# Optimization experiments

Hardware: AMD Instinct MI355X
Metric: run time of the kernel (lower is better)

## Reference

```python
import jax, jax.numpy as jnp
import numpy as np

B, N, C = 8, 4096, 3
IN_DIM = 2
HID = 512
NL = 256          # num_latents
DEPTH = 6
H, DH = 8, 64     # heads, dim_head (cross and latent)
INNER = H * DH
LAT = 32          # latent (bottleneck) dim
NF, MAXF = 12, 4  # NeRF num_freq, max_freq_log2
FF = 4 * HID
SCALE = DH ** -0.5
NERF_DIM = 2 * NF * IN_DIM  # 48


def layer_norm(x, g, b, eps=1e-5):
    m = jnp.mean(x, axis=-1, keepdims=True)
    v = jnp.mean((x - m) ** 2, axis=-1, keepdims=True)
    return (x - m) * jax.lax.rsqrt(v + eps) * g + b


def nerf_encode(pos):
    # log-sampled frequency bands: 2^linspace(0, MAXF, NF)
    freqs = 2.0 ** jnp.linspace(0.0, float(MAXF), NF)
    ang = pos[..., None] * freqs            # [B,N,IN_DIM,NF]
    enc = jnp.concatenate([jnp.sin(ang), jnp.cos(ang)], axis=-1)  # [B,N,IN_DIM,2NF]
    return enc.reshape(*pos.shape[:-1], NERF_DIM)


def mha(q, k, v):
    # q:[B,Nq,INNER] k,v:[B,Nk,INNER] -> [B,Nq,INNER]
    def split(t):
        b, n, _ = t.shape
        return t.reshape(b, n, H, DH).transpose(0, 2, 1, 3)  # [B,H,n,DH]
    qh, kh, vh = split(q), split(k), split(v)
    sim = jnp.einsum('bhid,bhjd->bhij', qh, kh) * SCALE
    attn = jax.nn.softmax(sim, axis=-1)
    o = jnp.einsum('bhij,bhjd->bhid', attn, vh)
    return o.transpose(0, 2, 1, 3).reshape(q.shape[0], q.shape[1], INNER)


def setup_inputs():
    key = jax.random.key(0)
    ks = iter(jax.random.split(key, 64))
    def w(*shape):
        return jax.random.normal(next(ks), shape, jnp.float32) * 0.02
    inp = {}
    inp['x'] = jax.random.normal(next(ks), (B, N, C), jnp.float32)
    inp['pos'] = jax.random.uniform(next(ks), (B, N, IN_DIM), jnp.float32)
    # input embeddings
    inp['W_pos'] = w(NERF_DIM, HID); inp['b_pos'] = jnp.zeros((HID,), jnp.float32)
    inp['W_in'] = w(C, HID); inp['b_in'] = jnp.zeros((HID,), jnp.float32)
    inp['latents'] = w(NL, HID)
    # cross-attention (PreNormCross: norm on q, k, v)
    for n in ('lnq', 'lnk', 'lnv'):
        inp[n + '_g'] = jnp.ones((HID,), jnp.float32)
        inp[n + '_b'] = jnp.zeros((HID,), jnp.float32)
    inp['cWq'] = w(HID, INNER); inp['cWk'] = w(HID, INNER); inp['cWv'] = w(HID, INNER)
    inp['cWo'] = w(INNER, HID); inp['c_bo'] = jnp.zeros((HID,), jnp.float32)
    # self-attention + FFN stacks
    inp['ln1_g'] = jnp.ones((DEPTH, HID), jnp.float32); inp['ln1_b'] = jnp.zeros((DEPTH, HID), jnp.float32)
    inp['sWq'] = w(DEPTH, HID, INNER); inp['sWkv'] = w(DEPTH, HID, 2 * INNER)
    inp['sWo'] = w(DEPTH, INNER, HID); inp['s_bo'] = jnp.zeros((DEPTH, HID), jnp.float32)
    inp['ln2_g'] = jnp.ones((DEPTH, HID), jnp.float32); inp['ln2_b'] = jnp.zeros((DEPTH, HID), jnp.float32)
    inp['fW1'] = w(DEPTH, HID, FF); inp['f_b1'] = jnp.zeros((DEPTH, FF), jnp.float32)
    inp['fW2'] = w(DEPTH, FF, HID); inp['f_b2'] = jnp.zeros((DEPTH, HID), jnp.float32)
    # final norm + gaussian bottleneck projection (mean, logvar)
    inp['lnf_g'] = jnp.ones((HID,), jnp.float32); inp['lnf_b'] = jnp.zeros((HID,), jnp.float32)
    inp['Wb'] = w(HID, 2 * LAT); inp['bb'] = jnp.zeros((2 * LAT,), jnp.float32)
    return inp


def reference(x, pos, W_pos, b_pos, W_in, b_in, latents,
              lnq_g, lnq_b, lnk_g, lnk_b, lnv_g, lnv_b,
              cWq, cWk, cWv, cWo, c_bo,
              ln1_g, ln1_b, sWq, sWkv, sWo, s_bo,
              ln2_g, ln2_b, fW1, f_b1, fW2, f_b2,
              lnf_g, lnf_b, Wb, bb):
    # positional embedding (FourierPositionalEmbedding with relu)
    kin = jax.nn.relu(nerf_encode(pos) @ W_pos + b_pos)   # [B,N,HID]
    vin = x @ W_in + b_in                                 # [B,N,HID]
    vin = vin + kin                                       # include_pos_in_value
    lat = jnp.broadcast_to(latents, (B, NL, HID))
    # cross-attention block (PreNormCross + residual)
    qn = layer_norm(lat, lnq_g, lnq_b)
    kn = layer_norm(kin, lnk_g, lnk_b)
    vn = layer_norm(vin, lnv_g, lnv_b)
    o = mha(qn @ cWq, kn @ cWk, vn @ cWv) @ cWo + c_bo
    lat = lat + o
    # latent self-attention + FFN blocks
    for i in range(DEPTH):
        h1 = layer_norm(lat, ln1_g[i], ln1_b[i])
        q = h1 @ sWq[i]
        k, v = jnp.split(h1 @ sWkv[i], 2, axis=-1)
        lat = lat + (mha(q, k, v) @ sWo[i] + s_bo[i])
        h2 = layer_norm(lat, ln2_g[i], ln2_b[i])
        lat = lat + (jax.nn.gelu(h2 @ fW1[i] + f_b1[i]) @ fW2[i] + f_b2[i])
    # bottleneck projection -> (mean | logvar)
    out = layer_norm(lat, lnf_g, lnf_b) @ Wb + bb         # [B,NL,2*LAT]
    return out
```

## Files before the change

### kernel.cpp

```cpp
#include <hip/hip_runtime.h>
#include <hip/hip_bf16.h>

#define DEV __device__ __forceinline__

typedef __attribute__((ext_vector_type(8))) short short8;
typedef __attribute__((ext_vector_type(4))) float floatx4;

DEV short f2bf(float f) {
  unsigned u = __float_as_uint(f);
  u += 0x7fffu + ((u >> 16) & 1u);
  return (short)(u >> 16);
}
DEV float bf2f(short s) {
  return __uint_as_float(((unsigned)(unsigned short)s) << 16);
}
DEV float wred(float v) {
#pragma unroll
  for (int m = 1; m < 64; m <<= 1) v += __shfl_xor(v, m);
  return v;
}
DEV floatx4 mfma16(short8 a, short8 b, floatx4 c) {
  return __builtin_amdgcn_mfma_f32_16x16x32_bf16(a, b, c, 0, 0, 0);
}
DEV void gload16(void* lds, const void* g) {
  __builtin_amdgcn_global_load_lds(
      (const __attribute__((address_space(1))) unsigned int*)g,
      (__attribute__((address_space(3))) unsigned int*)lds, 16, 0, 0);
}

struct MatDesc { const float* src; int K; int N; int kp; int off; float scale; };
struct MatTable { MatDesc m[36]; };

__global__ __launch_bounds__(256) void wtrans_kernel(MatTable T, short* __restrict__ dst) {
  int mi = blockIdx.y;
  MatDesc d = T.m[mi];
  int tilesx = d.N >> 5, tilesy = d.kp >> 5;
  int tb = blockIdx.x;
  if (tb >= tilesx * tilesy) return;
  int ty = tb / tilesx, tx = tb % tilesx;
  __shared__ float tile[32][33];
  int tid = threadIdx.x;
#pragma unroll
  for (int i = 0; i < 4; ++i) {
    int e = tid + i * 256, lr = e >> 5, lc = e & 31;
    int kk = ty * 32 + lr;
    tile[lr][lc] = (kk < d.K) ? d.src[(size_t)kk * d.N + tx * 32 + lc] : 0.f;
  }
  __syncthreads();
#pragma unroll
  for (int i = 0; i < 4; ++i) {
    int e = tid + i * 256, lr = e >> 5, lc = e & 31;
    dst[(size_t)d.off + (size_t)(tx * 32 + lr) * d.kp + ty * 32 + lc] =
        f2bf(tile[lc][lr] * d.scale);
  }
}

__global__ __launch_bounds__(256) void enc_kernel(const float* __restrict__ pos,
                                                  short* __restrict__ enc) {
  int idx = blockIdx.x * 256 + threadIdx.x;
  int row = idx >> 3, oct = idx & 7;
  float p0 = pos[row * 2], p1 = pos[row * 2 + 1];
  short8 o;
#pragma unroll
  for (int j = 0; j < 8; ++j) {
    int k = oct * 8 + j;
    float val = 0.f;
    if (k < 48) {
      int dd = k / 24, rem = k % 24;
      int trig = rem / 12, f = rem % 12;
      float ang = (dd ? p1 : p0) * exp2f((4.0f / 11.0f) * (float)f);
      val = trig ? __cosf(ang) : __sinf(ang);
    }
    o[j] = f2bf(val);
  }
  *(short8*)&enc[(size_t)row * 64 + oct * 8] = o;
}

#define LDA_S 516
__global__ __launch_bounds__(512) void embed2_kernel(
    const short* __restrict__ enc, const short* __restrict__ Wt,
    const float* __restrict__ b_pos, const float* __restrict__ W_in,
    const float* __restrict__ b_in, const float* __restrict__ x,
    const float* __restrict__ lnk_g, const float* __restrict__ lnk_b,
    const float* __restrict__ lnv_g, const float* __restrict__ lnv_b,
    short* __restrict__ kn, short* __restrict__ vn) {
  __shared__ short SS[128 * LDA_S];
  short* Wl = SS;
  short* El = SS + 32768;
  int tid = threadIdx.x;
  int lane = tid & 63, wv = tid >> 6;
  int c = lane & 15, g = lane >> 4;
  int blk = blockIdx.x * 128;
#pragma unroll
  for (int gi = 0; gi < 8; ++gi) {
    int grp = wv * 8 + gi;
    int row = grp * 8 + (lane >> 3), kc = lane & 7;
    gload16(&Wl[grp * 512], &Wt[(size_t)row * 64 + ((kc ^ (row & 7)) * 8)]);
  }
#pragma unroll
  for (int gi = 0; gi < 2; ++gi) {
    int grp = wv * 2 + gi;
    int row = grp * 8 + (lane >> 3), kc = lane & 7;
    gload16(&El[grp * 512], &enc[(size_t)(blk + row) * 64 + ((kc ^ (row & 7)) * 8)]);
  }
  __syncthreads();

  floatx4 acc[32];
  floatx4 zf = {0.f, 0.f, 0.f, 0.f};
#pragma unroll
  for (int nf = 0; nf < 32; ++nf) acc[nf] = zf;
  short8 af[2];
#pragma unroll
  for (int ks = 0; ks < 2; ++ks)
    af[ks] = *(const short8*)&El[(wv * 16 + c) * 64 + ((ks * 4 + g) ^ (c & 7)) * 8];
#pragma unroll
  for (int nf = 0; nf < 32; ++nf) {
#pragma unroll
    for (int ks = 0; ks < 2; ++ks) {
      short8 bf8 = *(const short8*)&Wl[(nf * 16 + c) * 64 + ((ks * 4 + g) ^ (c & 7)) * 8];
      acc[nf] = mfma16(af[ks], bf8, acc[nf]);
    }
  }

  int rowbase = blk + wv * 16 + g * 4;
  int lrow = wv * 16 + g * 4;
  float x0[4], x1[4], x2[4];
  float s1[4], q1[4], s2[4], q2[4];
#pragma unroll
  for (int r = 0; r < 4; ++r) {
    x0[r] = x[(size_t)(rowbase + r) * 3];
    x1[r] = x[(size_t)(rowbase + r) * 3 + 1];
    x2[r] = x[(size_t)(rowbase + r) * 3 + 2];
    s1[r] = 0; q1[r] = 0; s2[r] = 0; q2[r] = 0;
  }
#pragma unroll
  for (int nf = 0; nf < 32; ++nf) {
    int col = nf * 16 + c;
    float bp = b_pos[col];
    float w0 = W_in[col], w1 = W_in[512 + col], w2 = W_in[1024 + col], bi = b_in[col];
#pragma unroll
    for (int r = 0; r < 4; ++r) {
      float kk = fmaxf(acc[nf][r] + bp, 0.f);
      float vv = kk + x0[r] * w0 + x1[r] * w1 + x2[r] * w2 + bi;
      acc[nf][r] = kk;
      s1[r] += kk; q1[r] += kk * kk; s2[r] += vv; q2[r] += vv * vv;
    }
  }
  float m1[4], r1[4], m2[4], r2[4];
#pragma unroll
  for (int r = 0; r < 4; ++r) {
#pragma unroll
    for (int msk = 1; msk < 16; msk <<= 1) {
      s1[r] += __shfl_xor(s1[r], msk); q1[r] += __shfl_xor(q1[r], msk);
      s2[r] += __shfl_xor(s2[r], msk); q2[r] += __shfl_xor(q2[r], msk);
    }
    m1[r] = s1[r] * (1.f / 512.f);
    r1[r] = rsqrtf(q1[r] * (1.f / 512.f) - m1[r] * m1[r] + 1e-5f);
    m2[r] = s2[r] * (1.f / 512.f);
    r2[r] = rsqrtf(q2[r] * (1.f / 512.f) - m2[r] * m2[r] + 1e-5f);
  }
  __syncthreads();
#pragma unroll
  for (int nf = 0; nf < 32; ++nf) {
    int col = nf * 16 + c;
    float gk = lnk_g[col], bk = lnk_b[col];
#pragma unroll
    for (int r = 0; r < 4; ++r)
      SS[(lrow + r) * LDA_S + col] = f2bf((acc[nf][r] - m1[r]) * r1[r] * gk + bk);
  }
  __syncthreads();
#pragma unroll
  for (int it = 0; it < 16; ++it) {
    int e = it * 512 + tid;
    int row = e >> 6, colc = (e & 63) * 8;
    *(short8*)&kn[(size_t)(blk + row) * 512 + colc] = *(const short8*)&SS[row * LDA_S + colc];
  }
  __syncthreads();
#pragma unroll
  for (int nf = 0; nf < 32; ++nf) {
    int col = nf * 16 + c;
    float w0 = W_in[col], w1 = W_in[512 + col], w2 = W_in[1024 + col], bi = b_in[col];
    float gv = lnv_g[col], bv = lnv_b[col];
#pragma unroll
    for (int r = 0; r < 4; ++r) {
      float vv = acc[nf][r] + x0[r] * w0 + x1[r] * w1 + x2[r] * w2 + bi;
      SS[(lrow + r) * LDA_S + col] = f2bf((vv - m2[r]) * r2[r] * gv + bv);
    }
  }
  __syncthreads();
#pragma unroll
  for (int it = 0; it < 16; ++it) {
    int e = it * 512 + tid;
    int row = e >> 6, colc = (e & 63) * 8;
    *(short8*)&vn[(size_t)(blk + row) * 512 + colc] = *(const short8*)&SS[row * LDA_S + colc];
  }
}

__global__ __launch_bounds__(256) void ln_kernel(
    const float* __restrict__ in, const float* __restrict__ g,
    const float* __restrict__ b, short* __restrict__ out, int M) {
  int row = blockIdx.x * 4 + (threadIdx.x >> 6);
  if (row >= M) return;
  int lane = threadIdx.x & 63;
  float v[8]; float s = 0, q = 0;
#pragma unroll
  for (int j = 0; j < 8; ++j) {
    v[j] = in[(size_t)row * 512 + lane + 64 * j];
    s += v[j]; q += v[j] * v[j];
  }
  s = wred(s); q = wred(q);
  float m = s * (1.f / 512.f);
  float rs = rsqrtf(q * (1.f / 512.f) - m * m + 1e-5f);
#pragma unroll
  for (int j = 0; j < 8; ++j) {
    int cc = lane + 64 * j;
    out[(size_t)row * 512 + cc] = f2bf((v[j] - m) * rs * g[cc] + b[cc]);
  }
}

__global__ void bcast_kernel(const float* __restrict__ latents, float* __restrict__ lat) {
  int i = blockIdx.x * 256 + threadIdx.x;
  lat[i] = latents[i & 131071];
}

template <int EPI>
DEV void epi_store(void* outp, size_t idx, float xv) {
  if (EPI == 0) {
    ((short*)outp)[idx] = f2bf(xv);
  } else if (EPI == 1) {
    float t = 0.7978845608f * (xv + 0.044715f * xv * xv * xv);
    ((short*)outp)[idx] = f2bf(0.5f * xv * (1.f + tanhf(t)));
  } else if (EPI == 2) {
    ((float*)outp)[idx] += xv;
  } else {
    ((float*)outp)[idx] = xv;
  }
}

template <int EPI>
__global__ __launch_bounds__(256) void gemm_kernel(
    const short* __restrict__ A, const short* __restrict__ Wt,
    const float* __restrict__ bias, void* __restrict__ outp,
    int M, int N, int K, int lda, int ldo) {
  __shared__ short Alds[128 * 64];
  __shared__ short Blds[128 * 64];
  int tid = threadIdx.x;
  int brow = blockIdx.y * 128, bcol = blockIdx.x * 128;
  int lane = tid & 63, wvid = tid >> 6;
  int wr = wvid >> 1, wc = wvid & 1;
  int g = lane >> 4, c = lane & 15;
  floatx4 zf = {0.f, 0.f, 0.f, 0.f};
  floatx4 acc[4][4];
#pragma unroll
  for (int i = 0; i < 4; ++i)
#pragma unroll
    for (int j = 0; j < 4; ++j) acc[i][j] = zf;

  int srow = (lane >> 3), skc = lane & 7;
  for (int k0 = 0; k0 < K; k0 += 64) {
#pragma unroll
    for (int gi = 0; gi < 4; ++gi) {
      int grp = wvid * 4 + gi;
      int row = grp * 8 + srow;
      int sw = ((skc ^ (row & 7)) * 8);
      gload16(&Alds[grp * 512], &A[(size_t)(brow + row) * lda + k0 + sw]);
      gload16(&Blds[grp * 512], &Wt[(size_t)(bcol + row) * K + k0 + sw]);
    }
    __syncthreads();
#pragma unroll
    for (int ks = 0; ks < 2; ++ks) {
      int slot = ((ks * 4 + g) ^ (c & 7)) * 8;
      short8 af[4], bf8[4];
#pragma unroll
      for (int mf = 0; mf < 4; ++mf)
        af[mf] = *(const short8*)&Alds[(wr * 64 + mf * 16 + c) * 64 + slot];
#pragma unroll
      for (int nf = 0; nf < 4; ++nf)
        bf8[nf] = *(const short8*)&Blds[(wc * 64 + nf * 16 + c) * 64 + slot];
#pragma unroll
      for (int mf = 0; mf < 4; ++mf)
#pragma unroll
        for (int nf = 0; nf < 4; ++nf)
          acc[mf][nf] = mfma16(af[mf], bf8[nf], acc[mf][nf]);
    }
    __syncthreads();
  }

#pragma unroll
  for (int mf = 0; mf < 4; ++mf) {
#pragma unroll
    for (int nf = 0; nf < 4; ++nf) {
      int col = bcol + wc * 64 + nf * 16 + c;
      float bv = bias ? bias[col] : 0.f;
      int row0 = brow + wr * 64 + mf * 16 + g * 4;
#pragma unroll
      for (int r = 0; r < 4; ++r)
        epi_store<EPI>(outp, (size_t)(row0 + r) * ldo + col, acc[mf][nf][r] + bv);
    }
  }
}

template <int EPI>
__global__ __launch_bounds__(256) void gemm64_kernel(
    const short* __restrict__ A, const short* __restrict__ Wt,
    const float* __restrict__ bias, void* __restrict__ outp,
    int M, int N, int K, int lda, int ldo) {
  __shared__ short Alds[64 * 64];
  __shared__ short Blds[64 * 64];
  int tid = threadIdx.x;
  int brow = blockIdx.y * 64, bcol = blockIdx.x * 64;
  int lane = tid & 63, wvid = tid >> 6;
  int wr = wvid >> 1, wc = wvid & 1;
  int g = lane >> 4, c = lane & 15;
  floatx4 zf = {0.f, 0.f, 0.f, 0.f};
  floatx4 acc[2][2];
#pragma unroll
  for (int i = 0; i < 2; ++i)
#pragma unroll
    for (int j = 0; j < 2; ++j) acc[i][j] = zf;

  int srow = (lane >> 3), skc = lane & 7;
  for (int k0 = 0; k0 < K; k0 += 64) {
#pragma unroll
    for (int gi = 0; gi < 2; ++gi) {
      int grp = wvid * 2 + gi;
      int row = grp * 8 + srow;
      int sw = ((skc ^ (row & 7)) * 8);
      gload16(&Alds[grp * 512], &A[(size_t)(brow + row) * lda + k0 + sw]);
      gload16(&Blds[grp * 512], &Wt[(size_t)(bcol + row) * K + k0 + sw]);
    }
    __syncthreads();
#pragma unroll
    for (int ks = 0; ks < 2; ++ks) {
      int slot = ((ks * 4 + g) ^ (c & 7)) * 8;
      short8 af[2], bf8[2];
#pragma unroll
      for (int mf = 0; mf < 2; ++mf)
        af[mf] = *(const short8*)&Alds[(wr * 32 + mf * 16 + c) * 64 + slot];
#pragma unroll
      for (int nf = 0; nf < 2; ++nf)
        bf8[nf] = *(const short8*)&Blds[(wc * 32 + nf * 16 + c) * 64 + slot];
#pragma unroll
      for (int mf = 0; mf < 2; ++mf)
#pragma unroll
        for (int nf = 0; nf < 2; ++nf)
          acc[mf][nf] = mfma16(af[mf], bf8[nf], acc[mf][nf]);
    }
    __syncthreads();
  }

#pragma unroll
  for (int mf = 0; mf < 2; ++mf) {
#pragma unroll
    for (int nf = 0; nf < 2; ++nf) {
      int col = bcol + wc * 32 + nf * 16 + c;
      float bv = bias ? bias[col] : 0.f;
      int row0 = brow + wr * 32 + mf * 16 + g * 4;
#pragma unroll
      for (int r = 0; r < 4; ++r)
        epi_store<EPI>(outp, (size_t)(row0 + r) * ldo + col, acc[mf][nf][r] + bv);
    }
  }
}

__global__ __launch_bounds__(512) void flashsp_kernel(
    const short* __restrict__ q, const short* __restrict__ k,
    const short* __restrict__ v, float* __restrict__ po,
    float* __restrict__ pm, float* __restrict__ pl,
    int qrs, int qbrows, long kvbstride, int kvrstride,
    int seglen, int lognseg) {
  __shared__ short Qs[128 * 64];
  __shared__ short Ks[64 * 64];
  __shared__ short Vt[64 * 72];
  __shared__ short Ps[128 * 72];
  int tid = threadIdx.x;
  int bz = blockIdx.z;
  int b = bz >> lognseg, seg = bz & ((1 << lognseg) - 1);
  int h = blockIdx.y, qt = blockIdx.x;
  int lane = tid & 63, wv = tid >> 6;
  int g = lane >> 4, c = lane & 15;
  int srow = lane >> 3, skc = lane & 7;

#pragma unroll
  for (int gi = 0; gi < 2; ++gi) {
    int grp = wv * 2 + gi;
    int row = grp * 8 + srow;
    int sw = ((skc ^ (row & 7)) * 8);
    gload16(&Qs[grp * 512],
            &q[((size_t)(b * qbrows) + qt * 128 + row) * qrs + h * 64 + sw]);
  }

  float m_[4], l_[4];
  floatx4 zf = {0.f, 0.f, 0.f, 0.f};
  floatx4 o_[4];
#pragma unroll
  for (int r = 0; r < 4; ++r) { m_[r] = -3.0e38f; l_[r] = 0.f; }
#pragma unroll
  for (int f = 0; f < 4; ++f) o_[f] = zf;

  int tbeg = seg * seglen, tend = tbeg + seglen;
  for (int t0 = tbeg; t0 < tend; t0 += 64) {
    {
      int row = wv * 8 + srow;
      int sw = ((skc ^ (row & 7)) * 8);
      gload16(&Ks[wv * 512],
              &k[(size_t)b * kvbstride + (size_t)(t0 + row) * kvrstride + h * 64 + sw]);
    }
    {
      int j = tid >> 3, f0 = (tid & 7) * 8, mm = tid & 7, tg = j >> 3;
      short8 tv = *(const short8*)&v[(size_t)b * kvbstride + (size_t)(t0 + j) * kvrstride + h * 64 + f0];
#pragma unroll
      for (int jj = 0; jj < 8; ++jj)
        Vt[(f0 + jj) * 72 + ((tg ^ mm) * 8) + (j & 7)] = tv[jj];
    }
    __syncthreads();

    floatx4 s[4];
#pragma unroll
    for (int f = 0; f < 4; ++f) s[f] = zf;
#pragma unroll
    for (int ks = 0; ks < 2; ++ks) {
      int slot = ((ks * 4 + g) ^ (c & 7)) * 8;
      short8 a = *(const short8*)&Qs[(wv * 16 + c) * 64 + slot];
#pragma unroll
      for (int f = 0; f < 4; ++f) {
        short8 b8 = *(const short8*)&Ks[(f * 16 + c) * 64 + slot];
        s[f] = mfma16(a, b8, s[f]);
      }
    }

    float nm[4], sf[4], rs[4];
#pragma unroll
    for (int r = 0; r < 4; ++r) {
      float t = fmaxf(fmaxf(s[0][r], s[1][r]), fmaxf(s[2][r], s[3][r]));
#pragma unroll
      for (int msk = 1; msk < 16; msk <<= 1) t = fmaxf(t, __shfl_xor(t, msk));
      nm[r] = fmaxf(m_[r], t);
      sf[r] = __expf(m_[r] - nm[r]);
      rs[r] = 0.f;
    }
#pragma unroll
    for (int f = 0; f < 4; ++f)
#pragma unroll
      for (int r = 0; r < 4; ++r) {
        float p = __expf(s[f][r] - nm[r]);
        s[f][r] = p; rs[r] += p;
      }
#pragma unroll
    for (int r = 0; r < 4; ++r) {
#pragma unroll
      for (int msk = 1; msk < 16; msk <<= 1) rs[r] += __shfl_xor(rs[r], msk);
      l_[r] = l_[r] * sf[r] + rs[r];
      m_[r] = nm[r];
    }
#pragma unroll
    for (int f = 0; f < 4; ++f)
#pragma unroll
      for (int r = 0; r < 4; ++r) o_[f][r] *= sf[r];
#pragma unroll
    for (int f = 0; f < 4; ++f)
#pragma unroll
      for (int r = 0; r < 4; ++r)
        Ps[(wv * 16 + g * 4 + r) * 72 + f * 16 + c] = f2bf(s[f][r]);
    __syncthreads();
#pragma unroll
    for (int ks = 0; ks < 2; ++ks) {
      short8 pa = *(const short8*)&Ps[(wv * 16 + c) * 72 + ks * 32 + g * 8];
#pragma unroll
      for (int f = 0; f < 4; ++f) {
        int mm = (2 * f + (c >> 3)) & 7;
        short8 vb = *(const short8*)&Vt[(f * 16 + c) * 72 + ((ks * 4 + g) ^ mm) * 8];
        o_[f] = mfma16(pa, vb, o_[f]);
      }
    }
    __syncthreads();
  }

#pragma unroll
  for (int f = 0; f < 4; ++f)
#pragma unroll
    for (int r = 0; r < 4; ++r) {
      int row = qt * 128 + wv * 16 + g * 4 + r;
      size_t grow = (size_t)seg * 2048 + b * 256 + row;
      po[grow * 512 + h * 64 + f * 16 + c] = o_[f][r];
      if (f == 0 && c == 0) {
        pm[grow * 8 + h] = m_[r];
        pl[grow * 8 + h] = l_[r];
      }
    }
}

template <int NSEG>
__global__ __launch_bounds__(256) void fcomb_kernel(
    const float* __restrict__ po, const float* __restrict__ pm,
    const float* __restrict__ pl, short* __restrict__ out) {
  int idx = blockIdx.x * 256 + threadIdx.x;
  int grow = idx >> 9, col = idx & 511, h = col >> 6;
  float ms[NSEG];
  float M = -3.0e38f;
#pragma unroll
  for (int s = 0; s < NSEG; ++s) {
    ms[s] = pm[((size_t)s * 2048 + grow) * 8 + h];
    M = fmaxf(M, ms[s]);
  }
  float L = 0.f, acc = 0.f;
#pragma unroll
  for (int s = 0; s < NSEG; ++s) {
    float w = __expf(ms[s] - M);
    L += w * pl[((size_t)s * 2048 + grow) * 8 + h];
    acc += w * po[((size_t)s * 2048 + grow) * 512 + col];
  }
  out[idx] = f2bf(acc / L);
}

extern "C" void kernel_launch(void* const* d_in, const int* in_sizes, int n_in,
                              void* d_out, int out_size, void* d_ws, size_t ws_size,
                              hipStream_t stream) {
  const float* x       = (const float*)d_in[0];
  const float* pos     = (const float*)d_in[1];
  const float* W_pos   = (const float*)d_in[2];
  const float* b_pos   = (const float*)d_in[3];
  const float* W_in    = (const float*)d_in[4];
  const float* b_in    = (const float*)d_in[5];
  const float* latents = (const float*)d_in[6];
  const float* lnq_g   = (const float*)d_in[7];
  const float* lnq_b   = (const float*)d_in[8];
  const float* lnk_g   = (const float*)d_in[9];
  const float* lnk_b   = (const float*)d_in[10];
  const float* lnv_g   = (const float*)d_in[11];
  const float* lnv_b   = (const float*)d_in[12];
  const float* cWq     = (const float*)d_in[13];
  const float* cWk     = (const float*)d_in[14];
  const float* cWv     = (const float*)d_in[15];
  const float* cWo     = (const float*)d_in[16];
  const float* c_bo    = (const float*)d_in[17];
  const float* ln1_g   = (const float*)d_in[18];
  const float* ln1_b   = (const float*)d_in[19];
  const float* sWq     = (const float*)d_in[20];
  const float* sWkv    = (const float*)d_in[21];
  const float* sWo     = (const float*)d_in[22];
  const float* s_bo    = (const float*)d_in[23];
  const float* ln2_g   = (const float*)d_in[24];
  const float* ln2_b   = (const float*)d_in[25];
  const float* fW1     = (const float*)d_in[26];
  const float* f_b1    = (const float*)d_in[27];
  const float* fW2     = (const float*)d_in[28];
  const float* f_b2    = (const float*)d_in[29];
  const float* lnf_g   = (const float*)d_in[30];
  const float* lnf_b   = (const float*)d_in[31];
  const float* Wb      = (const float*)d_in[32];
  const float* bbv     = (const float*)d_in[33];
  float* outp = (float*)d_out;

  size_t W = 0;
  size_t o_cWq = W; W += 512 * 512;
  size_t o_cWk = W; W += 512 * 512;
  size_t o_cWv = W; W += 512 * 512;
  size_t o_cWo = W; W += 512 * 512;
  size_t o_Wb  = W; W += 64 * 512;
  size_t o_Wpos = W; W += 512 * 64;
  size_t o_sQKV[6], o_sWo[6], o_fW1[6], o_fW2[6];
  for (int i = 0; i < 6; ++i) {
    o_sQKV[i] = W; W += 1536 * 512;
    o_sWo[i]  = W; W += 512 * 512;
    o_fW1[i]  = W; W += 2048 * 512;
    o_fW2[i]  = W; W += 512 * 2048;
  }
  MatTable T;
  int nm = 0;
  auto add = [&](const float* s, int K, int N, int kp, size_t off, float sc) {
    T.m[nm].src = s; T.m[nm].K = K; T.m[nm].N = N; T.m[nm].kp = kp;
    T.m[nm].off = (int)off; T.m[nm].scale = sc; ++nm;
  };
  const float SC = 0.125f;
  add(cWq, 512, 512, 512, o_cWq, SC); add(cWk, 512, 512, 512, o_cWk, 1.f);
  add(cWv, 512, 512, 512, o_cWv, 1.f); add(cWo, 512, 512, 512, o_cWo, 1.f);
  add(Wb, 512, 64, 512, o_Wb, 1.f);
  add(W_pos, 48, 512, 64, o_Wpos, 1.f);
  for (int i = 0; i < 6; ++i) {
    add(sWq  + (size_t)i * 512 * 512,  512, 512,  512, o_sQKV[i], SC);
    add(sWkv + (size_t)i * 512 * 1024, 512, 1024, 512, o_sQKV[i] + 512 * 512, 1.f);
    add(sWo  + (size_t)i * 512 * 512,  512, 512,  512, o_sWo[i], 1.f);
    add(fW1  + (size_t)i * 512 * 2048, 512, 2048, 512, o_fW1[i], 1.f);
    add(fW2  + (size_t)i * 2048 * 512, 2048, 512, 2048, o_fW2[i], 1.f);
  }

  char* p = (char*)d_ws;
  auto carve = [&](size_t bytes) {
    char* r = p; p += (bytes + 255) & ~(size_t)255; return r;
  };
  short* wtb   = (short*)carve(W * 2);
  short* enc   = (short*)carve((size_t)32768 * 64 * 2);
  short* kn    = (short*)carve(33554432);
  short* vn    = (short*)carve(33554432);
  short* kvc   = (short*)carve((size_t)32768 * 1024 * 2);
  short* latn0 = (short*)carve(262144);
  short* qc    = (short*)carve(262144);
  float* lat   = (float*)carve(4194304);
  float* pm    = (float*)carve(1048576);
  float* pl    = (float*)carve(1048576);
  short* attno = enc;
  float* po    = (float*)kn;
  short* h     = (short*)((char*)kn + 36 * 1048576);
  short* qkv   = (short*)((char*)kn + 40 * 1048576);
  short* ffh   = (short*)((char*)kn + 48 * 1048576);

  wtrans_kernel<<<dim3(1024, 36), 256, 0, stream>>>(T, wtb);
  enc_kernel<<<1024, 256, 0, stream>>>(pos, enc);
  embed2_kernel<<<256, 512, 0, stream>>>(enc, wtb + o_Wpos, b_pos, W_in, b_in, x,
                                         lnk_g, lnk_b, lnv_g, lnv_b, kn, vn);
  bcast_kernel<<<4096, 256, 0, stream>>>(latents, lat);
  ln_kernel<<<64, 256, 0, stream>>>(latents, lnq_g, lnq_b, latn0, 256);
  gemm64_kernel<0><<<dim3(8, 4), 256, 0, stream>>>(latn0, wtb + o_cWq, nullptr, qc, 256, 512, 512, 512, 512);
  gemm_kernel<0><<<dim3(4, 256), 256, 0, stream>>>(kn, wtb + o_cWk, nullptr, kvc, 32768, 512, 512, 512, 1024);
  gemm_kernel<0><<<dim3(4, 256), 256, 0, stream>>>(vn, wtb + o_cWv, nullptr, kvc + 512, 32768, 512, 512, 512, 1024);
  flashsp_kernel<<<dim3(2, 8, 64), 512, 0, stream>>>(qc, kvc, kvc + 512, po, pm, pl,
                                                     512, 0, (long)4096 * 1024, 1024, 512, 3);
  fcomb_kernel<8><<<4096, 256, 0, stream>>>(po, pm, pl, attno);
  gemm64_kernel<2><<<dim3(8, 32), 256, 0, stream>>>(attno, wtb + o_cWo, c_bo, lat, 2048, 512, 512, 512, 512);

  for (int i = 0; i < 6; ++i) {
    ln_kernel<<<512, 256, 0, stream>>>(lat, ln1_g + i * 512, ln1_b + i * 512, h, 2048);
    gemm64_kernel<0><<<dim3(24, 32), 256, 0, stream>>>(h, wtb + o_sQKV[i], nullptr, qkv, 2048, 1536, 512, 512, 1536);
    flashsp_kernel<<<dim3(2, 8, 32), 512, 0, stream>>>(qkv, qkv + 512, qkv + 1024, po, pm, pl,
                                                       1536, 256, (long)256 * 1536, 1536, 64, 2);
    fcomb_kernel<4><<<4096, 256, 0, stream>>>(po, pm, pl, attno);
    gemm64_kernel<2><<<dim3(8, 32), 256, 0, stream>>>(attno, wtb + o_sWo[i], s_bo + i * 512, lat, 2048, 512, 512, 512, 512);
    ln_kernel<<<512, 256, 0, stream>>>(lat, ln2_g + i * 512, ln2_b + i * 512, h, 2048);
    gemm64_kernel<1><<<dim3(32, 32), 256, 0, stream>>>(h, wtb + o_fW1[i], f_b1 + i * 2048, ffh, 2048, 2048, 512, 512, 2048);
    gemm64_kernel<2><<<dim3(8, 32), 256, 0, stream>>>(ffh, wtb + o_fW2[i], f_b2 + i * 512, lat, 2048, 512, 2048, 2048, 512);
  }
  ln_kernel<<<512, 256, 0, stream>>>(lat, lnf_g, lnf_b, h, 2048);
  gemm64_kernel<3><<<dim3(1, 32), 256, 0, stream>>>(h, wtb + o_Wb, bbv, outp, 2048, 64, 512, 512, 64);
}
```

Baseline: 822.6 us.

## Fuse LayerNorm into GEMM A-loads and shrink embed LDS staging buffer

Adds a gemm64ln kernel that computes per-row LayerNorm statistics from the fp32 input, then normalizes and converts A tiles to bf16 on the fly while loading them into LDS. This removes the separate ln_kernel launches and the bf16 intermediate round trips before the Q, QKV, FFN1 and bottleneck GEMMs. Each block recomputes the row stats and rereads fp32 A instead of bf16, which is redundant work across column blocks. The embed kernel also stages its output in two 64-row halves so it uses a smaller LDS buffer, which could allow higher occupancy, at the cost of extra barriers.

```diff
diff --git a/kernel.cpp b/kernel.cpp
--- a/kernel.cpp
+++ b/kernel.cpp
@@ -13,11 +13,6 @@
 }
 DEV float bf2f(short s) {
   return __uint_as_float(((unsigned)(unsigned short)s) << 16);
-}
-DEV float wred(float v) {
-#pragma unroll
-  for (int m = 1; m < 64; m <<= 1) v += __shfl_xor(v, m);
-  return v;
 }
 DEV floatx4 mfma16(short8 a, short8 b, floatx4 c) {
   return __builtin_amdgcn_mfma_f32_16x16x32_bf16(a, b, c, 0, 0, 0);
@@ -76,7 +71,7 @@
   *(short8*)&enc[(size_t)row * 64 + oct * 8] = o;
 }
 
-#define LDA_S 516
+#define LDA_S 528
 __global__ __launch_bounds__(512) void embed2_kernel(
     const short* __restrict__ enc, const short* __restrict__ Wt,
     const float* __restrict__ b_pos, const float* __restrict__ W_in,
@@ -84,7 +79,7 @@
     const float* __restrict__ lnk_g, const float* __restrict__ lnk_b,
     const float* __restrict__ lnv_g, const float* __restrict__ lnv_b,
     short* __restrict__ kn, short* __restrict__ vn) {
-  __shared__ short SS[128 * LDA_S];
+  __shared__ short SS[40960];
   short* Wl = SS;
   short* El = SS + 32768;
   int tid = threadIdx.x;
@@ -123,7 +118,6 @@
   }
 
   int rowbase = blk + wv * 16 + g * 4;
-  int lrow = wv * 16 + g * 4;
   float x0[4], x1[4], x2[4];
   float s1[4], q1[4], s2[4], q2[4];
 #pragma unroll
@@ -159,62 +153,55 @@
     m2[r] = s2[r] * (1.f / 512.f);
     r2[r] = rsqrtf(q2[r] * (1.f / 512.f) - m2[r] * m2[r] + 1e-5f);
   }
-  __syncthreads();
-#pragma unroll
-  for (int nf = 0; nf < 32; ++nf) {
-    int col = nf * 16 + c;
-    float gk = lnk_g[col], bk = lnk_b[col];
-#pragma unroll
-    for (int r = 0; r < 4; ++r)
-      SS[(lrow + r) * LDA_S + col] = f2bf((acc[nf][r] - m1[r]) * r1[r] * gk + bk);
-  }
-  __syncthreads();
-#pragma unroll
-  for (int it = 0; it < 16; ++it) {
-    int e = it * 512 + tid;
-    int row = e >> 6, colc = (e & 63) * 8;
-    *(short8*)&kn[(size_t)(blk + row) * 512 + colc] = *(const short8*)&SS[row * LDA_S + colc];
-  }
-  __syncthreads();
-#pragma unroll
-  for (int nf = 0; nf < 32; ++nf) {
-    int col = nf * 16 + c;
-    float w0 = W_in[col], w1 = W_in[512 + col], w2 = W_in[1024 + col], bi = b_in[col];
-    float gv = lnv_g[col], bv = lnv_b[col];
-#pragma unroll
-    for (int r = 0; r < 4; ++r) {
-      float vv = acc[nf][r] + x0[r] * w0 + x1[r] * w1 + x2[r] * w2 + bi;
-      SS[(lrow + r) * LDA_S + col] = f2bf((vv - m2[r]) * r2[r] * gv + bv);
-    }
-  }
-  __syncthreads();
-#pragma unroll
-  for (int it = 0; it < 16; ++it) {
-    int e = it * 512 + tid;
-    int row = e >> 6, colc = (e & 63) * 8;
-    *(short8*)&vn[(size_t)(blk + row) * 512 + colc] = *(const short8*)&SS[row * LDA_S + colc];
-  }
-}
-
-__global__ __launch_bounds__(256) void ln_kernel(
-    const float* __restrict__ in, const float* __restrict__ g,
-    const float* __restrict__ b, short* __restrict__ out, int M) {
-  int row = blockIdx.x * 4 + (threadIdx.x >> 6);
-  if (row >= M) return;
-  int lane = threadIdx.x & 63;
-  float v[8]; float s = 0, q = 0;
-#pragma unroll
-  for (int j = 0; j < 8; ++j) {
-    v[j] = in[(size_t)row * 512 + lane + 64 * j];
-    s += v[j]; q += v[j] * v[j];
-  }
-  s = wred(s); q = wred(q);
-  float m = s * (1.f / 512.f);
-  float rs = rsqrtf(q * (1.f / 512.f) - m * m + 1e-5f);
-#pragma unroll
-  for (int j = 0; j < 8; ++j) {
-    int cc = lane + 64 * j;
-    out[(size_t)row * 512 + cc] = f2bf((v[j] - m) * rs * g[cc] + b[cc]);
+
+  int halfsel = wv >> 2;
+  int lrow = (wv & 3) * 16 + g * 4;
+#pragma unroll
+  for (int half = 0; half < 2; ++half) {
+    __syncthreads();
+    if (halfsel == half) {
+#pragma unroll
+      for (int nf = 0; nf < 32; ++nf) {
+        int col = nf * 16 + c;
+        float gk = lnk_g[col], bk = lnk_b[col];
+#pragma unroll
+        for (int r = 0; r < 4; ++r)
+          SS[(lrow + r) * LDA_S + col] = f2bf((acc[nf][r] - m1[r]) * r1[r] * gk + bk);
+      }
+    }
+    __syncthreads();
+    int gbase = blk + half * 64;
+#pragma unroll
+    for (int it = 0; it < 8; ++it) {
+      int e = it * 512 + tid;
+      int row = e >> 6, colc = (e & 63) * 8;
+      *(short8*)&kn[(size_t)(gbase + row) * 512 + colc] = *(const short8*)&SS[row * LDA_S + colc];
+    }
+  }
+#pragma unroll
+  for (int half = 0; half < 2; ++half) {
+    __syncthreads();
+    if (halfsel == half) {
+#pragma unroll
+      for (int nf = 0; nf < 32; ++nf) {
+        int col = nf * 16 + c;
+        float w0 = W_in[col], w1 = W_in[512 + col], w2 = W_in[1024 + col], bi = b_in[col];
+        float gv = lnv_g[col], bv = lnv_b[col];
+#pragma unroll
+        for (int r = 0; r < 4; ++r) {
+          float vv = acc[nf][r] + x0[r] * w0 + x1[r] * w1 + x2[r] * w2 + bi;
+          SS[(lrow + r) * LDA_S + col] = f2bf((vv - m2[r]) * r2[r] * gv + bv);
+        }
+      }
+    }
+    __syncthreads();
+    int gbase = blk + half * 64;
+#pragma unroll
+    for (int it = 0; it < 8; ++it) {
+      int e = it * 512 + tid;
+      int row = e >> 6, colc = (e & 63) * 8;
+      *(short8*)&vn[(size_t)(gbase + row) * 512 + colc] = *(const short8*)&SS[row * LDA_S + colc];
+    }
   }
 }
 
@@ -328,6 +315,113 @@
       int sw = ((skc ^ (row & 7)) * 8);
       gload16(&Alds[grp * 512], &A[(size_t)(brow + row) * lda + k0 + sw]);
       gload16(&Blds[grp * 512], &Wt[(size_t)(bcol + row) * K + k0 + sw]);
+    }
+    __syncthreads();
+#pragma unroll
+    for (int ks = 0; ks < 2; ++ks) {
+      int slot = ((ks * 4 + g) ^ (c & 7)) * 8;
+      short8 af[2], bf8[2];
+#pragma unroll
+      for (int mf = 0; mf < 2; ++mf)
+        af[mf] = *(const short8*)&Alds[(wr * 32 + mf * 16 + c) * 64 + slot];
+#pragma unroll
+      for (int nf = 0; nf < 2; ++nf)
+        bf8[nf] = *(const short8*)&Blds[(wc * 32 + nf * 16 + c) * 64 + slot];
+#pragma unroll
+      for (int mf = 0; mf < 2; ++mf)
+#pragma unroll
+        for (int nf = 0; nf < 2; ++nf)
+          acc[mf][nf] = mfma16(af[mf], bf8[nf], acc[mf][nf]);
+    }
+    __syncthreads();
+  }
+
+#pragma unroll
+  for (int mf = 0; mf < 2; ++mf) {
+#pragma unroll
+    for (int nf = 0; nf < 2; ++nf) {
+      int col = bcol + wc * 32 + nf * 16 + c;
+      float bv = bias ? bias[col] : 0.f;
+      int row0 = brow + wr * 32 + mf * 16 + g * 4;
+#pragma unroll
+      for (int r = 0; r < 4; ++r)
+        epi_store<EPI>(outp, (size_t)(row0 + r) * ldo + col, acc[mf][nf][r] + bv);
+    }
+  }
+}
+
+template <int EPI>
+__global__ __launch_bounds__(256) void gemm64ln_kernel(
+    const float* __restrict__ A, const short* __restrict__ Wt,
+    const float* __restrict__ lg, const float* __restrict__ lb,
+    const float* __restrict__ bias, void* __restrict__ outp,
+    int M, int N, int ldo) {
+  __shared__ short Alds[64 * 64];
+  __shared__ short Blds[64 * 64];
+  __shared__ float stats[128];
+  int tid = threadIdx.x;
+  int brow = blockIdx.y * 64, bcol = blockIdx.x * 64;
+  int lane = tid & 63, wvid = tid >> 6;
+  int wr = wvid >> 1, wc = wvid & 1;
+  int g = lane >> 4, c = lane & 15;
+
+  {
+    int row = tid >> 2, seg = tid & 3;
+    const float* ap = &A[(size_t)(brow + row) * 512 + seg * 128];
+    float s = 0.f, q = 0.f;
+#pragma unroll
+    for (int i = 0; i < 32; ++i) {
+      floatx4 v = *(const floatx4*)&ap[i * 4];
+      s += v[0] + v[1] + v[2] + v[3];
+      q += v[0] * v[0] + v[1] * v[1] + v[2] * v[2] + v[3] * v[3];
+    }
+    s += __shfl_xor(s, 1); s += __shfl_xor(s, 2);
+    q += __shfl_xor(q, 1); q += __shfl_xor(q, 2);
+    if (seg == 0) {
+      float m = s * (1.f / 512.f);
+      stats[row] = m;
+      stats[64 + row] = rsqrtf(q * (1.f / 512.f) - m * m + 1e-5f);
+    }
+  }
+  __syncthreads();
+
+  floatx4 zf = {0.f, 0.f, 0.f, 0.f};
+  floatx4 acc[2][2];
+#pragma unroll
+  for (int i = 0; i < 2; ++i)
+#pragma unroll
+    for (int j = 0; j < 2; ++j) acc[i][j] = zf;
+
+  int srow = lane >> 3, skc = lane & 7;
+  int arow = tid >> 2, akc2 = (tid & 3) * 2;
+  float am = stats[arow], ars = stats[64 + arow];
+
+  for (int k0 = 0; k0 < 512; k0 += 64) {
+#pragma unroll
+    for (int kk = 0; kk < 2; ++kk) {
+      int kc = akc2 + kk;
+      int cb = k0 + kc * 8;
+      floatx4 v0 = *(const floatx4*)&A[(size_t)(brow + arow) * 512 + cb];
+      floatx4 v1 = *(const floatx4*)&A[(size_t)(brow + arow) * 512 + cb + 4];
+      floatx4 g0 = *(const floatx4*)&lg[cb];
+      floatx4 g1 = *(const floatx4*)&lg[cb + 4];
+      floatx4 b0 = *(const floatx4*)&lb[cb];
+      floatx4 b1 = *(const floatx4*)&lb[cb + 4];
+      short8 o;
+#pragma unroll
+      for (int j = 0; j < 4; ++j) {
+        o[j]     = f2bf((v0[j] - am) * ars * g0[j] + b0[j]);
+        o[4 + j] = f2bf((v1[j] - am) * ars * g1[j] + b1[j]);
+      }
+      int slot = kc ^ (arow & 7);
+      *(short8*)&Alds[arow * 64 + slot * 8] = o;
+    }
+#pragma unroll
+    for (int gi = 0; gi < 2; ++gi) {
+      int grp = wvid * 2 + gi;
+      int row = grp * 8 + srow;
+      int sw = ((skc ^ (row & 7)) * 8);
+      gload16(&Blds[grp * 512], &Wt[(size_t)(bcol + row) * 512 + k0 + sw]);
     }
     __syncthreads();
 #pragma unroll
@@ -594,14 +688,12 @@
   short* kn    = (short*)carve(33554432);
   short* vn    = (short*)carve(33554432);
   short* kvc   = (short*)carve((size_t)32768 * 1024 * 2);
-  short* latn0 = (short*)carve(262144);
   short* qc    = (short*)carve(262144);
   float* lat   = (float*)carve(4194304);
   float* pm    = (float*)carve(1048576);
   float* pl    = (float*)carve(1048576);
   short* attno = enc;
   float* po    = (float*)kn;
-  short* h     = (short*)((char*)kn + 36 * 1048576);
   short* qkv   = (short*)((char*)kn + 40 * 1048576);
   short* ffh   = (short*)((char*)kn + 48 * 1048576);
 
@@ -610,8 +702,8 @@
   embed2_kernel<<<256, 512, 0, stream>>>(enc, wtb + o_Wpos, b_pos, W_in, b_in, x,
                                          lnk_g, lnk_b, lnv_g, lnv_b, kn, vn);
   bcast_kernel<<<4096, 256, 0, stream>>>(latents, lat);
-  ln_kernel<<<64, 256, 0, stream>>>(latents, lnq_g, lnq_b, latn0, 256);
-  gemm64_kernel<0><<<dim3(8, 4), 256, 0, stream>>>(latn0, wtb + o_cWq, nullptr, qc, 256, 512, 512, 512, 512);
+  gemm64ln_kernel<0><<<dim3(8, 4), 256, 0, stream>>>(latents, wtb + o_cWq, lnq_g, lnq_b,
+                                                     nullptr, qc, 256, 512, 512);
   gemm_kernel<0><<<dim3(4, 256), 256, 0, stream>>>(kn, wtb + o_cWk, nullptr, kvc, 32768, 512, 512, 512, 1024);
   gemm_kernel<0><<<dim3(4, 256), 256, 0, stream>>>(vn, wtb + o_cWv, nullptr, kvc + 512, 32768, 512, 512, 512, 1024);
   flashsp_kernel<<<dim3(2, 8, 64), 512, 0, stream>>>(qc, kvc, kvc + 512, po, pm, pl,
@@ -620,16 +712,18 @@
   gemm64_kernel<2><<<dim3(8, 32), 256, 0, stream>>>(attno, wtb + o_cWo, c_bo, lat, 2048, 512, 512, 512, 512);
 
   for (int i = 0; i < 6; ++i) {
-    ln_kernel<<<512, 256, 0, stream>>>(lat, ln1_g + i * 512, ln1_b + i * 512, h, 2048);
-    gemm64_kernel<0><<<dim3(24, 32), 256, 0, stream>>>(h, wtb + o_sQKV[i], nullptr, qkv, 2048, 1536, 512, 512, 1536);
+    gemm64ln_kernel<0><<<dim3(24, 32), 256, 0, stream>>>(lat, wtb + o_sQKV[i],
+                                                         ln1_g + i * 512, ln1_b + i * 512,
+                                                         nullptr, qkv, 2048, 1536, 1536);
     flashsp_kernel<<<dim3(2, 8, 32), 512, 0, stream>>>(qkv, qkv + 512, qkv + 1024, po, pm, pl,
                                                        1536, 256, (long)256 * 1536, 1536, 64, 2);
     fcomb_kernel<4><<<4096, 256, 0, stream>>>(po, pm, pl, attno);
     gemm64_kernel<2><<<dim3(8, 32), 256, 0, stream>>>(attno, wtb + o_sWo[i], s_bo + i * 512, lat, 2048, 512, 512, 512, 512);
-    ln_kernel<<<512, 256, 0, stream>>>(lat, ln2_g + i * 512, ln2_b + i * 512, h, 2048);
-    gemm64_kernel<1><<<dim3(32, 32), 256, 0, stream>>>(h, wtb + o_fW1[i], f_b1 + i * 2048, ffh, 2048, 2048, 512, 512, 2048);
+    gemm64ln_kernel<1><<<dim3(32, 32), 256, 0, stream>>>(lat, wtb + o_fW1[i],
+                                                         ln2_g + i * 512, ln2_b + i * 512,
+                                                         f_b1 + i * 2048, ffh, 2048, 2048, 2048);
     gemm64_kernel<2><<<dim3(8, 32), 256, 0, stream>>>(ffh, wtb + o_fW2[i], f_b2 + i * 512, lat, 2048, 512, 2048, 2048, 512);
   }
-  ln_kernel<<<512, 256, 0, stream>>>(lat, lnf_g, lnf_b, h, 2048);
-  gemm64_kernel<3><<<dim3(1, 32), 256, 0, stream>>>(h, wtb + o_Wb, bbv, outp, 2048, 64, 512, 512, 64);
-}
+  gemm64ln_kernel<3><<<dim3(1, 32), 256, 0, stream>>>(lat, wtb + o_Wb, lnf_g, lnf_b,
+                                                      bbv, outp, 2048, 64, 64);
+}
```

Measured after the change: 1.146 ms. 39.3% more time.
